# Performance work log

Measured on AMD Instinct MI355X. Metric: run time of the kernel, lower is better.

Reference implementation:

```python
import jax, jax.numpy as jnp
import numpy as np

N = 65536          # total detections
PER = 64           # boxes per frame (max_per_img)
B = N // PER       # frames
NUM_CLASSES = 36   # len(obj_classes), incl. background
OBJ_DIM = 192
EMB = 200
POS = 128
HID = 1024
EPS = 1e-5


def setup_inputs() -> dict:
    key = jax.random.key(0)
    ks = jax.random.split(key, 16)
    # distribution: per-box class scores over 35 foreground classes
    distribution = jax.random.uniform(ks[0], (N, NUM_CLASSES - 1), jnp.float32)
    features = jax.random.normal(ks[1], (N, OBJ_DIM), jnp.float32)
    # boxes: [img_idx, x1, y1, x2, y2], 64 boxes per frame, img_idx sorted
    img_idx = (jnp.arange(N) // PER).astype(jnp.float32)
    xy1 = jax.random.uniform(ks[2], (N, 2), jnp.float32) * 500.0
    wh = jax.random.uniform(ks[3], (N, 2), jnp.float32) * 100.0 + 1.0
    boxes = jnp.concatenate([img_idx[:, None], xy1, xy1 + wh], axis=1)
    # parameters
    obj_embed_W = jax.random.normal(ks[4], (NUM_CLASSES - 1, EMB), jnp.float32) * 0.1
    bn4_g = jnp.ones((4,), jnp.float32)
    bn4_b = jnp.zeros((4,), jnp.float32)
    bn4_m = jnp.zeros((4,), jnp.float32)
    bn4_v = jnp.ones((4,), jnp.float32)
    pos_W = jax.random.normal(ks[5], (4, POS), jnp.float32) * 0.05
    pos_b = jnp.zeros((POS,), jnp.float32)
    dec1_W = jax.random.normal(ks[6], (OBJ_DIM + EMB + POS, HID), jnp.float32) * 0.02
    dec1_b = jnp.zeros((HID,), jnp.float32)
    bn1k_g = jnp.ones((HID,), jnp.float32)
    bn1k_b = jnp.zeros((HID,), jnp.float32)
    bn1k_m = jnp.zeros((HID,), jnp.float32)
    bn1k_v = jnp.ones((HID,), jnp.float32)
    dec2_W = jax.random.normal(ks[7], (HID, NUM_CLASSES), jnp.float32) * 0.02
    dec2_b = jnp.zeros((NUM_CLASSES,), jnp.float32)
    return dict(distribution=distribution, features=features, boxes=boxes,
                obj_embed_W=obj_embed_W, bn4_g=bn4_g, bn4_b=bn4_b, bn4_m=bn4_m, bn4_v=bn4_v,
                pos_W=pos_W, pos_b=pos_b, dec1_W=dec1_W, dec1_b=dec1_b,
                bn1k_g=bn1k_g, bn1k_b=bn1k_b, bn1k_m=bn1k_m, bn1k_v=bn1k_v,
                dec2_W=dec2_W, dec2_b=dec2_b)


def reference(distribution, features, boxes, obj_embed_W, bn4_g, bn4_b, bn4_m, bn4_v,
              pos_W, pos_b, dec1_W, dec1_b, bn1k_g, bn1k_b, bn1k_m, bn1k_v,
              dec2_W, dec2_b):
    # soft object-class embedding: [N,35] @ [35,200]
    obj_embed = distribution @ obj_embed_W
    # center_size(boxes[:,1:]): (cx, cy, w, h)
    xy1 = boxes[:, 1:3]
    xy2 = boxes[:, 3:5]
    wh = xy2 - xy1 + 1.0
    cs = jnp.concatenate([xy1 + 0.5 * wh, wh], axis=1)
    # pos_embed: BatchNorm1d(4) (eval) -> Linear(4,128) -> ReLU (dropout=id in eval)
    h = (cs - bn4_m) * jax.lax.rsqrt(bn4_v + EPS) * bn4_g + bn4_b
    pos = jax.nn.relu(h @ pos_W + pos_b)
    # decoder_lin: Linear(520,1024) -> BN(1024, eval) -> ReLU -> Linear(1024,36)
    obj_feat = jnp.concatenate([features, obj_embed, pos], axis=1)  # [N,520]
    g = obj_feat @ dec1_W + dec1_b
    g = (g - bn1k_m) * jax.lax.rsqrt(bn1k_v + EPS) * bn1k_g + bn1k_b
    g = jax.nn.relu(g)
    logits = g @ dec2_W + dec2_b  # [N,36]
    # drop background, softmax over foreground classes
    dist = jax.nn.softmax(logits[:, 1:], axis=1)  # [N,35]
    pred_scores = jnp.max(dist[:, 1:], axis=1)
    pred_labels = jnp.argmax(dist[:, 1:], axis=1) + 2
    # per-frame human argmax over class-0 (human) score; 64 boxes per frame
    human_local = jnp.argmax(dist[:, 0].reshape(B, PER), axis=1)
    human_idx = jnp.arange(B) * PER + human_local  # [B]
    pred_labels = pred_labels.at[human_idx].set(1)
    pred_scores = pred_scores.at[human_idx].set(dist[human_idx, 0])
    return dist, pred_scores, pred_labels, human_idx
```

## Files before the change

kernel.cpp:

```cpp
#include <hip/hip_runtime.h>
#include <math.h>

#define NROWS 65536
#define PER 64
#define BIMG 1024
#define NCLS 36
#define OBJ_DIM 192
#define EMB 200
#define POSD 128
#define HID 1024
#define EPSV 1e-5f

#define KP 384
#define XSTR 392
#define LSTR 52


typedef __attribute__((ext_vector_type(8))) _Float16 f16x8;
typedef __attribute__((ext_vector_type(4))) _Float16 f16x4;
typedef __attribute__((ext_vector_type(4))) float f32x4;

__global__ __launch_bounds__(256) void k_fold(
    const float* __restrict__ obj_embed_W, const float* __restrict__ dec1_W,
    float* __restrict__ Fold)
{
    int e = blockIdx.x;
    int h = blockIdx.y * 256 + threadIdx.x;
    const float* A  = obj_embed_W + (size_t)e * EMB;
    const float* Bp = dec1_W + (size_t)192 * HID + h;
    float acc = 0.f;
#pragma unroll 8
    for (int j = 0; j < EMB; ++j)
        acc = fmaf(A[j], Bp[(size_t)j * HID], acc);
    Fold[(size_t)e * HID + h] = acc;
}

__global__ __launch_bounds__(256) void k_prep(
    const float* __restrict__ Fold, const float* __restrict__ dec1_W,
    const float* __restrict__ dec1_b,
    const float* __restrict__ bn1k_g, const float* __restrict__ bn1k_b,
    const float* __restrict__ bn1k_m, const float* __restrict__ bn1k_v,
    const float* __restrict__ dec2_W,
    _Float16* __restrict__ W1p, _Float16* __restrict__ W2p,
    float* __restrict__ bs)
{
    int idx = blockIdx.x * 256 + threadIdx.x;
    if (idx < HID * KP) {
        int e  = idx & 7;
        int l  = (idx >> 3) & 63;
        int ks = (idx >> 9) % 12;
        int ht = idx / 6144;
        int h = ht * 16 + (l & 15);
        int k = ks * 32 + (l >> 4) * 8 + e;
        float sc = rsqrtf(bn1k_v[h] + EPSV) * bn1k_g[h];
        float v;
        if (k < 192)      v = dec1_W[(size_t)k * HID + h];
        else if (k < 320) v = dec1_W[(size_t)(k + 200) * HID + h];
        else if (k < 355) v = Fold[(size_t)(k - 320) * HID + h];
        else              v = 0.f;
        W1p[idx] = (_Float16)(v * sc);
        if (k == 0) bs[h] = (dec1_b[h] - bn1k_m[h]) * sc + bn1k_b[h];
    } else {
        int p2 = idx - HID * KP;
        if (p2 < 64 * 3 * 256) {
            int e   = p2 & 3;
            int l   = (p2 >> 2) & 63;
            int cls = (p2 >> 8) % 3;
            int ht  = p2 / 768;
            int h = 16 * ht + 4 * (l >> 4) + e;
            int c = 16 * cls + (l & 15);
            W2p[p2] = (c < NCLS) ? (_Float16)dec2_W[(size_t)h * NCLS + c] : (_Float16)0.f;
        }
    }
}

__global__ __launch_bounds__(512, 4) void k_main(
    const float* __restrict__ distribution, const float* __restrict__ features,
    const float* __restrict__ boxes,
    const float* __restrict__ bn4_g, const float* __restrict__ bn4_b,
    const float* __restrict__ bn4_m, const float* __restrict__ bn4_v,
    const float* __restrict__ pos_W, const float* __restrict__ pos_b,
    const _Float16* __restrict__ W1p, const _Float16* __restrict__ W2p,
    const float* __restrict__ bs, const float* __restrict__ dec2_b,
    float* __restrict__ out)
{
    __shared__ __align__(16) char smem[53248];
    _Float16* Xs = (_Float16*)smem;
    float* Lst   = (float*)smem;

    int t = threadIdx.x;
    int row0 = blockIdx.x * PER;
    int wv = t >> 6, lane = t & 63, lr = lane & 15, lq = lane >> 4;

    {
        const f32x4* F4 = (const f32x4*)(features + (size_t)row0 * OBJ_DIM);
#pragma unroll
        for (int it = 0; it < 6; ++it) {
            int li = t + 512 * it;
            int r = li / 48, c4 = li % 48;
            f32x4 v = __builtin_nontemporal_load(F4 + li);
            f16x4 h4;
            h4[0] = (_Float16)v[0]; h4[1] = (_Float16)v[1];
            h4[2] = (_Float16)v[2]; h4[3] = (_Float16)v[3];
            *(f16x4*)&Xs[r * XSTR + c4 * 4] = h4;
        }
        const float* D = distribution + (size_t)row0 * (NCLS - 1);
        {
            int r = t >> 3, gq = t & 7;
            f16x8 v8;
#pragma unroll
            for (int e = 0; e < 8; ++e) {
                int c = gq * 8 + e;
                v8[e] = (c < 35) ? (_Float16)__builtin_nontemporal_load(D + (size_t)r * 35 + c)
                                 : (_Float16)0.f;
            }
            *(f16x8*)&Xs[r * XSTR + 320 + gq * 8] = v8;
        }
        int r = t >> 3, kq = t & 7;
        int grow = row0 + r;
        const float* bx = boxes + (size_t)grow * 5;
        float x1 = bx[1], y1 = bx[2], x2 = bx[3], y2 = bx[4];
        float w = x2 - x1 + 1.f, hh = y2 - y1 + 1.f;
        float cs[4] = {x1 + 0.5f * w, y1 + 0.5f * hh, w, hh};
        float hv[4];
#pragma unroll
        for (int i = 0; i < 4; i++)
            hv[i] = (cs[i] - bn4_m[i]) * rsqrtf(bn4_v[i] + EPSV) * bn4_g[i] + bn4_b[i];
#pragma unroll
        for (int jb = 0; jb < 2; ++jb) {
            int j0 = kq * 16 + jb * 8;
            f16x8 v8;
#pragma unroll
            for (int e = 0; e < 8; ++e) {
                int j = j0 + e;
                float p = pos_b[j];
                p = fmaf(hv[0], pos_W[j], p);
                p = fmaf(hv[1], pos_W[POSD + j], p);
                p = fmaf(hv[2], pos_W[2 * POSD + j], p);
                p = fmaf(hv[3], pos_W[3 * POSD + j], p);
                v8[e] = (_Float16)fmaxf(p, 0.f);
            }
            *(f16x8*)&Xs[r * XSTR + 192 + j0] = v8;
        }
    }
    __syncthreads();

    f32x4 Lg[4][3];
#pragma unroll
    for (int n = 0; n < 4; n++)
#pragma unroll
        for (int cls = 0; cls < 3; cls++) Lg[n][cls] = (f32x4){0.f, 0.f, 0.f, 0.f};

    for (int c0 = 0; c0 < 2; ++c0) {
        const _Float16* ap = W1p + ((size_t)(32 * c0 + wv) * 12) * 512 + (size_t)lane * 8;

        f32x4 C[4][4];
#pragma unroll
        for (int j = 0; j < 4; j++)
#pragma unroll
            for (int n = 0; n < 4; n++) C[j][n] = (f32x4){0.f, 0.f, 0.f, 0.f};

#pragma unroll 4
        for (int ks = 0; ks < 12; ++ks) {
            f16x8 ah[4], bh[4];
#pragma unroll
            for (int j = 0; j < 4; j++)
                ah[j] = *(const f16x8*)(ap + ((size_t)(8 * j) * 12 + ks) * 512);
#pragma unroll
            for (int n = 0; n < 4; n++)
                bh[n] = *(const f16x8*)&Xs[(16 * n + lr) * XSTR + ks * 32 + lq * 8];
#pragma unroll
            for (int j = 0; j < 4; j++)
#pragma unroll
                for (int n = 0; n < 4; n++)
                    C[j][n] = __builtin_amdgcn_mfma_f32_16x16x32_f16(ah[j], bh[n], C[j][n], 0, 0, 0);
        }

#pragma unroll
        for (int j = 0; j < 4; ++j) {
            int ht = 32 * c0 + wv + 8 * j;
            f32x4 bsv = *(const f32x4*)(bs + 16 * ht + 4 * lq);
            f16x4 af[4];
#pragma unroll
            for (int n = 0; n < 4; n++)
#pragma unroll
                for (int e = 0; e < 4; ++e)
                    af[n][e] = (_Float16)fmaxf(C[j][n][e] + bsv[e], 0.f);
#pragma unroll
            for (int cls = 0; cls < 3; ++cls) {
                f16x4 bf = *(const f16x4*)(W2p + ((size_t)(ht * 3 + cls) * 64 + lane) * 4);
#pragma unroll
                for (int n = 0; n < 4; n++)
                    Lg[n][cls] = __builtin_amdgcn_mfma_f32_16x16x16f16(af[n], bf, Lg[n][cls], 0, 0, 0);
            }
        }
    }

    __syncthreads();
    {
        float* Lw = Lst + (size_t)(wv & 3) * 64 * LSTR;
        if (wv < 4) {
#pragma unroll
            for (int n = 0; n < 4; n++)
#pragma unroll
                for (int cls = 0; cls < 3; cls++)
#pragma unroll
                    for (int e = 0; e < 4; ++e)
                        Lw[(16 * n + 4 * lq + e) * LSTR + 16 * cls + lr] = Lg[n][cls][e];
        }
        __syncthreads();
        if (wv >= 4) {
#pragma unroll
            for (int n = 0; n < 4; n++)
#pragma unroll
                for (int cls = 0; cls < 3; cls++)
#pragma unroll
                    for (int e = 0; e < 4; ++e)
                        Lw[(16 * n + 4 * lq + e) * LSTR + 16 * cls + lr] += Lg[n][cls][e];
        }
    }
    __syncthreads();

    if (t < 64) {
        int row = row0 + t;
        float lg[36];
#pragma unroll
        for (int c = 1; c < 36; ++c)
            lg[c] = Lst[t * LSTR + c] + Lst[64 * LSTR + t * LSTR + c]
                  + Lst[128 * LSTR + t * LSTR + c] + Lst[192 * LSTR + t * LSTR + c]
                  + dec2_b[c];
        float m = lg[1];
#pragma unroll
        for (int c = 2; c < 36; ++c) m = fmaxf(m, lg[c]);
        float d[35];
        float s = 0.f;
#pragma unroll
        for (int c = 1; c < 36; ++c) { float e = expf(lg[c] - m); d[c - 1] = e; s += e; }
        float inv = 1.0f / s;
        float* dout = out + (size_t)row * 35;
#pragma unroll
        for (int j = 0; j < 35; ++j) dout[j] = d[j] * inv;

        float best = -1.f; int bi = 1;
#pragma unroll
        for (int c = 1; c < 35; ++c) {
            float v = d[c] * inv;
            if (v > best) { best = v; bi = c; }
        }

        float v0 = d[0] * inv;
        float mv = v0; int mi = t;
#pragma unroll
        for (int off = 32; off > 0; off >>= 1) {
            float ov = __shfl_down(mv, off);
            int   oi = __shfl_down(mi, off);
            if (ov > mv || (ov == mv && oi < mi)) { mv = ov; mi = oi; }
        }
        int human = __shfl(mi, 0);
        bool isH = (t == human);
        out[(size_t)NROWS * 35 + row] = isH ? v0 : best;
        out[(size_t)NROWS * 36 + row] = isH ? 1.0f : (float)(bi + 1);
        if (t == 0) out[(size_t)NROWS * 37 + blockIdx.x] = (float)(row0 + human);
    }
}

extern "C" void kernel_launch(void* const* d_in, const int* in_sizes, int n_in,
                              void* d_out, int out_size, void* d_ws, size_t ws_size,
                              hipStream_t stream)
{
    (void)in_sizes; (void)n_in; (void)out_size; (void)ws_size;
    const float* distribution = (const float*)d_in[0];
    const float* features     = (const float*)d_in[1];
    const float* boxes        = (const float*)d_in[2];
    const float* obj_embed_W  = (const float*)d_in[3];
    const float* bn4_g        = (const float*)d_in[4];
    const float* bn4_b        = (const float*)d_in[5];
    const float* bn4_m        = (const float*)d_in[6];
    const float* bn4_v        = (const float*)d_in[7];
    const float* pos_W        = (const float*)d_in[8];
    const float* pos_b        = (const float*)d_in[9];
    const float* dec1_W       = (const float*)d_in[10];
    const float* dec1_b       = (const float*)d_in[11];
    const float* bn1k_g       = (const float*)d_in[12];
    const float* bn1k_b       = (const float*)d_in[13];
    const float* bn1k_m       = (const float*)d_in[14];
    const float* bn1k_v       = (const float*)d_in[15];
    const float* dec2_W       = (const float*)d_in[16];
    const float* dec2_b       = (const float*)d_in[17];

    float* out = (float*)d_out;

    _Float16* W1p  = (_Float16*)d_ws;
    _Float16* W2p  = W1p + (size_t)HID * KP;
    float*    bsv  = (float*)(W2p + (size_t)64 * 3 * 256);
    float*    Fold = bsv + HID;

    k_fold<<<dim3(35, 4), 256, 0, stream>>>(obj_embed_W, dec1_W, Fold);

    int prep_elems = HID * KP + 64 * 3 * 256;
    k_prep<<<(prep_elems + 255) / 256, 256, 0, stream>>>(
        Fold, dec1_W, dec1_b, bn1k_g, bn1k_b, bn1k_m, bn1k_v, dec2_W,
        W1p, W2p, bsv);

    k_main<<<BIMG, 512, 0, stream>>>(
        distribution, features, boxes, bn4_g, bn4_b, bn4_m, bn4_v, pos_W, pos_b,
        W1p, W2p, bsv, dec2_b, out);
}
```

Baseline: 234.4 us.

## Split waves across row halves to drop cross-wave logit reduction pass

Warps are regrouped so four hidden-column slices are each paired with one of two row halves, instead of all eight warps covering all 64 rows over disjoint hidden slices. Each warp now holds half as many accumulators, and the two-phase store-then-add reduction of logits in shared memory becomes a single direct store. This removes one barrier and the read-modify-write pass. In exchange, each warp loads W1 tiles for twice as many hidden tiles, so global and L2 weight traffic per block doubles, while shared-memory reads of the activation tile are halved.

Result: slower. 250.2 us (+6.7%).

```diff
diff --git a/kernel.cpp b/kernel.cpp
--- a/kernel.cpp
+++ b/kernel.cpp
@@ -91,6 +91,7 @@
     int t = threadIdx.x;
     int row0 = blockIdx.x * PER;
     int wv = t >> 6, lane = t & 63, lr = lane & 15, lq = lane >> 4;
+    int s = wv & 3, g = wv >> 2;
 
     {
         const f32x4* F4 = (const f32x4*)(features + (size_t)row0 * OBJ_DIM);
@@ -145,79 +146,67 @@
     }
     __syncthreads();
 
-    f32x4 Lg[4][3];
-#pragma unroll
-    for (int n = 0; n < 4; n++)
-#pragma unroll
-        for (int cls = 0; cls < 3; cls++) Lg[n][cls] = (f32x4){0.f, 0.f, 0.f, 0.f};
-
-    for (int c0 = 0; c0 < 2; ++c0) {
-        const _Float16* ap = W1p + ((size_t)(32 * c0 + wv) * 12) * 512 + (size_t)lane * 8;
-
-        f32x4 C[4][4];
+    f32x4 Lg[2][3];
+#pragma unroll
+    for (int nn = 0; nn < 2; nn++)
+#pragma unroll
+        for (int cls = 0; cls < 3; cls++) Lg[nn][cls] = (f32x4){0.f, 0.f, 0.f, 0.f};
+
+    for (int c0 = 0; c0 < 4; ++c0) {
+        const _Float16* ap = W1p + ((size_t)(16 * c0 + s) * 12) * 512 + (size_t)lane * 8;
+
+        f32x4 C[4][2];
 #pragma unroll
         for (int j = 0; j < 4; j++)
 #pragma unroll
-            for (int n = 0; n < 4; n++) C[j][n] = (f32x4){0.f, 0.f, 0.f, 0.f};
+            for (int nn = 0; nn < 2; nn++) C[j][nn] = (f32x4){0.f, 0.f, 0.f, 0.f};
 
 #pragma unroll 4
         for (int ks = 0; ks < 12; ++ks) {
-            f16x8 ah[4], bh[4];
+            f16x8 ah[4], bh[2];
 #pragma unroll
             for (int j = 0; j < 4; j++)
-                ah[j] = *(const f16x8*)(ap + ((size_t)(8 * j) * 12 + ks) * 512);
-#pragma unroll
-            for (int n = 0; n < 4; n++)
-                bh[n] = *(const f16x8*)&Xs[(16 * n + lr) * XSTR + ks * 32 + lq * 8];
+                ah[j] = *(const f16x8*)(ap + ((size_t)(4 * j) * 12 + ks) * 512);
+#pragma unroll
+            for (int nn = 0; nn < 2; nn++)
+                bh[nn] = *(const f16x8*)&Xs[(16 * (2 * g + nn) + lr) * XSTR + ks * 32 + lq * 8];
 #pragma unroll
             for (int j = 0; j < 4; j++)
 #pragma unroll
-                for (int n = 0; n < 4; n++)
-                    C[j][n] = __builtin_amdgcn_mfma_f32_16x16x32_f16(ah[j], bh[n], C[j][n], 0, 0, 0);
+                for (int nn = 0; nn < 2; nn++)
+                    C[j][nn] = __builtin_amdgcn_mfma_f32_16x16x32_f16(ah[j], bh[nn], C[j][nn], 0, 0, 0);
         }
 
 #pragma unroll
         for (int j = 0; j < 4; ++j) {
-            int ht = 32 * c0 + wv + 8 * j;
+            int ht = 16 * c0 + s + 4 * j;
             f32x4 bsv = *(const f32x4*)(bs + 16 * ht + 4 * lq);
-            f16x4 af[4];
-#pragma unroll
-            for (int n = 0; n < 4; n++)
+            f16x4 af[2];
+#pragma unroll
+            for (int nn = 0; nn < 2; nn++)
 #pragma unroll
                 for (int e = 0; e < 4; ++e)
-                    af[n][e] = (_Float16)fmaxf(C[j][n][e] + bsv[e], 0.f);
+                    af[nn][e] = (_Float16)fmaxf(C[j][nn][e] + bsv[e], 0.f);
 #pragma unroll
             for (int cls = 0; cls < 3; ++cls) {
                 f16x4 bf = *(const f16x4*)(W2p + ((size_t)(ht * 3 + cls) * 64 + lane) * 4);
 #pragma unroll
-                for (int n = 0; n < 4; n++)
-                    Lg[n][cls] = __builtin_amdgcn_mfma_f32_16x16x16f16(af[n], bf, Lg[n][cls], 0, 0, 0);
+                for (int nn = 0; nn < 2; nn++)
+                    Lg[nn][cls] = __builtin_amdgcn_mfma_f32_16x16x16f16(af[nn], bf, Lg[nn][cls], 0, 0, 0);
             }
         }
     }
 
     __syncthreads();
     {
-        float* Lw = Lst + (size_t)(wv & 3) * 64 * LSTR;
-        if (wv < 4) {
-#pragma unroll
-            for (int n = 0; n < 4; n++)
-#pragma unroll
-                for (int cls = 0; cls < 3; cls++)
-#pragma unroll
-                    for (int e = 0; e < 4; ++e)
-                        Lw[(16 * n + 4 * lq + e) * LSTR + 16 * cls + lr] = Lg[n][cls][e];
-        }
-        __syncthreads();
-        if (wv >= 4) {
-#pragma unroll
-            for (int n = 0; n < 4; n++)
-#pragma unroll
-                for (int cls = 0; cls < 3; cls++)
-#pragma unroll
-                    for (int e = 0; e < 4; ++e)
-                        Lw[(16 * n + 4 * lq + e) * LSTR + 16 * cls + lr] += Lg[n][cls][e];
-        }
+        float* Lw = Lst + (size_t)s * 64 * LSTR;
+#pragma unroll
+        for (int nn = 0; nn < 2; nn++)
+#pragma unroll
+            for (int cls = 0; cls < 3; cls++)
+#pragma unroll
+                for (int e = 0; e < 4; ++e)
+                    Lw[(16 * (2 * g + nn) + 4 * lq + e) * LSTR + 16 * cls + lr] = Lg[nn][cls][e];
     }
     __syncthreads();
 
@@ -233,10 +222,10 @@
 #pragma unroll
         for (int c = 2; c < 36; ++c) m = fmaxf(m, lg[c]);
         float d[35];
-        float s = 0.f;
-#pragma unroll
-        for (int c = 1; c < 36; ++c) { float e = expf(lg[c] - m); d[c - 1] = e; s += e; }
-        float inv = 1.0f / s;
+        float s2 = 0.f;
+#pragma unroll
+        for (int c = 1; c < 36; ++c) { float e = expf(lg[c] - m); d[c - 1] = e; s2 += e; }
+        float inv = 1.0f / s2;
         float* dout = out + (size_t)row * 35;
 #pragma unroll
         for (int j = 0; j < 35; ++j) dout[j] = d[j] * inv;
```
